# Kernel tuning notes

Hardware: AMD Instinct MI355X
Metric: run time of the kernel (lower is better)

The kernel has to match this reference:

```python
import math
import jax, jax.numpy as jnp
import numpy as np

DIM = 1280
NUM_HEADS = 16
HEAD_DIM = DIM // NUM_HEADS  # 80
N_SEG = 8
SEG_LEN = 1024
TOTAL = N_SEG * SEG_LEN  # 8192


def setup_inputs() -> dict:
    key = jax.random.key(0)
    ks = jax.random.split(key, 6)
    hidden_states = jax.random.normal(ks[0], (TOTAL, DIM), dtype=jnp.float32)
    # equal-length packed segments (8 images x 1024 patches)
    cu_seqlens = jnp.arange(N_SEG + 1, dtype=jnp.int32) * SEG_LEN
    rotary_pos_emb = jax.random.uniform(ks[1], (TOTAL, HEAD_DIM // 2), dtype=jnp.float32) * (2.0 * math.pi)
    s = 0.02
    qkv_w = jax.random.normal(ks[2], (DIM, 3 * DIM), dtype=jnp.float32) * s
    qkv_b = jnp.zeros((3 * DIM,), dtype=jnp.float32)
    proj_w = jax.random.normal(ks[3], (DIM, DIM), dtype=jnp.float32) * s
    proj_b = jnp.zeros((DIM,), dtype=jnp.float32)
    return {
        "hidden_states": hidden_states,
        "rotary_pos_emb": rotary_pos_emb,
        "qkv_w": qkv_w,
        "qkv_b": qkv_b,
        "proj_w": proj_w,
        "proj_b": proj_b,
        "cu_seqlens": cu_seqlens,
    }


def _rotate_half(x):
    d = x.shape[-1] // 2
    return jnp.concatenate([-x[..., d:], x[..., :d]], axis=-1)


def _apply_rope(t, freqs):
    # t: [S, H, D] ; freqs: [S, D/2]
    orig = t.dtype
    tf = t.astype(jnp.float32)
    cos = jnp.tile(jnp.cos(freqs), (1, 2))[:, None, :].astype(jnp.float32)  # [S,1,D]
    sin = jnp.tile(jnp.sin(freqs), (1, 2))[:, None, :].astype(jnp.float32)
    return (tf * cos + _rotate_half(tf) * sin).astype(orig)


def reference(hidden_states, rotary_pos_emb, qkv_w, qkv_b, proj_w, proj_b, cu_seqlens):
    S, dim = hidden_states.shape
    H, D = NUM_HEADS, HEAD_DIM
    n_seg = cu_seqlens.shape[0] - 1  # static
    L = S // n_seg  # equal-length segments

    qkv = hidden_states @ qkv_w + qkv_b            # [S, 3*dim]
    qkv = qkv.reshape(S, 3, H, D)
    q, k, v = qkv[:, 0], qkv[:, 1], qkv[:, 2]      # [S, H, D]

    q = _apply_rope(q, rotary_pos_emb)
    k = _apply_rope(k, rotary_pos_emb)

    # block-diagonal (per-segment) attention, vectorized over segments
    qs = q.reshape(n_seg, L, H, D).transpose(0, 2, 1, 3)  # [G,H,L,D]
    ks = k.reshape(n_seg, L, H, D).transpose(0, 2, 1, 3)
    vs = v.reshape(n_seg, L, H, D).transpose(0, 2, 1, 3)

    scale = 1.0 / math.sqrt(D)
    scores = jnp.einsum("ghld,ghmd->ghlm", qs, ks) * scale       # [G,H,L,L]
    probs = jax.nn.softmax(scores.astype(jnp.float32), axis=-1).astype(qs.dtype)
    out = jnp.einsum("ghlm,ghmd->ghld", probs, vs)               # [G,H,L,D]
    out = out.transpose(0, 2, 1, 3).reshape(S, H * D)            # [S, dim]
    return out @ proj_w + proj_b
```

## Files before the change

kernel.cpp:

```cpp
#include <hip/hip_runtime.h>
#include <hip/hip_bf16.h>
#include <math.h>

#define DIM 1280
#define NHEADS 16
#define HD 80
#define HDP 96
#define NSEG 8
#define SEGLEN 1024
#define TOTAL (NSEG*SEGLEN)

typedef unsigned short u16;
typedef __attribute__((ext_vector_type(8))) short bf16x8;
typedef __attribute__((ext_vector_type(4))) float f32x4;

__device__ __forceinline__ u16 f2b(float f) {
    union { float f; unsigned int i; } v; v.f = f;
    unsigned int x = v.i;
    unsigned int r = x + 0x7FFFu + ((x >> 16) & 1u);
    return (u16)(r >> 16);
}
__device__ __forceinline__ float b2f(u16 u) {
    union { unsigned int i; float f; } v; v.i = ((unsigned int)u) << 16;
    return v.f;
}
__device__ __forceinline__ void gload16(const u16* g, u16* l) {
    __builtin_amdgcn_global_load_lds(
        (const __attribute__((address_space(1))) unsigned int*)g,
        (__attribute__((address_space(3))) unsigned int*)l, 16, 0, 0);
}

__global__ __launch_bounds__(256) void cvt_f32_bf16(const float* __restrict__ in,
                                                    u16* __restrict__ out, int n4) {
    int i = blockIdx.x * 256 + threadIdx.x;
    if (i >= n4) return;
    float4 a = ((const float4*)in)[i];
    u16 o[4] = { f2b(a.x), f2b(a.y), f2b(a.z), f2b(a.w) };
    *(ulong1*)&out[i*4] = *(ulong1*)o;
}

__global__ __launch_bounds__(256) void cvtT_w(const float* __restrict__ in,
                                              u16* __restrict__ out, int K, int N) {
    __shared__ float t[32][33];
    const int kb = blockIdx.x * 32, nb = blockIdx.y * 32;
    const int tx = threadIdx.x & 31, ty = threadIdx.x >> 5;
    #pragma unroll
    for (int i = 0; i < 4; ++i) {
        int r = i*8 + ty;
        t[r][tx] = in[(size_t)(kb + r)*N + nb + tx];
    }
    __syncthreads();
    #pragma unroll
    for (int i = 0; i < 4; ++i) {
        int n = i*8 + ty;
        out[(size_t)(nb + n)*K + kb + tx] = f2b(t[tx][n]);
    }
}

template<int MODE>
__global__ __launch_bounds__(256) void gemm_bf16(
    const u16* __restrict__ A, const u16* __restrict__ BT,
    const float* __restrict__ bias,
    float* __restrict__ Cf, u16* __restrict__ qo, u16* __restrict__ ko,
    u16* __restrict__ vo, int M, int N, int K)
{
    __shared__ u16 sA[128*32];
    __shared__ u16 sB[128*32];
    const int tid = threadIdx.x;
    const int w = tid >> 6, l = tid & 63;
    const int lq = l & 15, lg = l >> 4;
    const int brow = blockIdx.y * 128, bcol = blockIdx.x * 128;
    const int wr = (w >> 1) * 64, wc = (w & 1) * 64;
    const int arow = w*32 + (l >> 2);
    const int acol = (l & 3) * 8;

    f32x4 acc[4][4] = {};

    for (int k0 = 0; k0 < K; k0 += 32) {
        __syncthreads();
        #pragma unroll
        for (int i = 0; i < 2; ++i) {
            gload16(A  + (size_t)(brow + arow + i*16)*K + k0 + acol, &sA[w*1024 + i*512]);
            gload16(BT + (size_t)(bcol + arow + i*16)*K + k0 + acol, &sB[w*1024 + i*512]);
        }
        __syncthreads();
        bf16x8 af[4], bfr[4];
        #pragma unroll
        for (int m = 0; m < 4; ++m) af[m]  = *(const bf16x8*)&sA[(wr + m*16 + lq)*32 + lg*8];
        #pragma unroll
        for (int n = 0; n < 4; ++n) bfr[n] = *(const bf16x8*)&sB[(wc + n*16 + lq)*32 + lg*8];
        #pragma unroll
        for (int m = 0; m < 4; ++m)
            #pragma unroll
            for (int n = 0; n < 4; ++n)
                acc[m][n] = __builtin_amdgcn_mfma_f32_16x16x32_bf16(af[m], bfr[n], acc[m][n], 0, 0, 0);
    }

    #pragma unroll
    for (int m = 0; m < 4; ++m) {
        #pragma unroll
        for (int n = 0; n < 4; ++n) {
            #pragma unroll
            for (int r = 0; r < 4; ++r) {
                const int row = brow + wr + m*16 + lg*4 + r;
                const int col = bcol + wc + n*16 + lq;
                float val = acc[m][n][r] + bias[col];
                if (MODE == 0) {
                    Cf[(size_t)row*N + col] = val;
                } else {
                    int part = col / DIM, rem = col - part*DIM;
                    int hh = rem / HD, dd = rem - hh*HD;
                    int g = row >> 10, ll = row & 1023;
                    size_t tok = (size_t)((g*NHEADS + hh)*SEGLEN + ll);
                    if      (part == 0) qo[tok*HDP + dd] = f2b(val);
                    else if (part == 1) ko[tok*HDP + dd] = f2b(val);
                    else                vo[tok*HD  + dd] = f2b(val);
                }
            }
        }
    }
}

__global__ __launch_bounds__(256) void rope_pad(u16* __restrict__ qb, u16* __restrict__ kb,
                                                const float* __restrict__ rp)
{
    int idx = blockIdx.x * 256 + threadIdx.x;
    int d = idx % 48;
    int t = idx / 48;
    int l = t & 1023, h = (t >> 10) & 15, g = t >> 14;
    size_t base = ((size_t)((g*NHEADS + h)*SEGLEN + l)) * HDP;
    if (d < 40) {
        float ang = rp[(size_t)(g*SEGLEN + l)*40 + d];
        float si, co;
        sincosf(ang, &si, &co);
        float q0 = b2f(qb[base + d]), q1 = b2f(qb[base + d + 40]);
        qb[base + d]      = f2b(q0*co - q1*si);
        qb[base + d + 40] = f2b(q1*co + q0*si);
        float k0 = b2f(kb[base + d]), k1 = b2f(kb[base + d + 40]);
        kb[base + d]      = f2b(k0*co - k1*si);
        kb[base + d + 40] = f2b(k1*co + k0*si);
    } else {
        int dz = d - 40;
        qb[base + 80 + dz] = 0; qb[base + 88 + dz] = 0;
        kb[base + 80 + dz] = 0; kb[base + 88 + dz] = 0;
    }
}

__global__ __launch_bounds__(256) void transpose_v(const u16* __restrict__ v,
                                                   u16* __restrict__ vt)
{
    __shared__ u16 sT[64][82];
    const int gh = blockIdx.y;
    const int st = blockIdx.x;
    const u16* src = v  + (size_t)gh*SEGLEN*HD + (size_t)st*64*HD;
    u16*       dst = vt + (size_t)gh*HD*SEGLEN + (size_t)st*64;
    const int tid = threadIdx.x;
    #pragma unroll
    for (int p = 0; p < 20; ++p) {
        int e = p*256 + tid;
        int r = e / 80, c = e - r*80;
        sT[r][c] = src[r*HD + c];
    }
    __syncthreads();
    #pragma unroll
    for (int p = 0; p < 20; ++p) {
        int e = p*256 + tid;
        int dd = e >> 6, s = e & 63;
        dst[(size_t)dd*SEGLEN + s] = sT[s][dd];
    }
}

__global__ __launch_bounds__(256) void attn_mfma(
    const u16* __restrict__ qb, const u16* __restrict__ kb,
    const u16* __restrict__ vt, u16* __restrict__ ob)
{
    const int qt = blockIdx.x;
    const int h  = blockIdx.y;
    const int g  = blockIdx.z;
    const float scale = 0.11180339887498949f;
    const float L2E = 1.4426950408889634f;

    __shared__ u16 sK[64*HDP];
    __shared__ u16 sVT[80][72];
    __shared__ u16 sP[4][16][72];

    const int tid = threadIdx.x;
    const int w = tid >> 6, l = tid & 63;
    const int lq = l & 15, lg = l >> 4;

    const size_t gh = (size_t)(g*NHEADS + h);
    const u16* Qg  = qb + gh*SEGLEN*HDP + (size_t)qt*64*HDP;
    const u16* Kg  = kb + gh*SEGLEN*HDP;
    const u16* VTg = vt + gh*HD*SEGLEN;

    bf16x8 qf[3];
    #pragma unroll
    for (int s = 0; s < 3; ++s)
        qf[s] = *(const bf16x8*)(Qg + (size_t)(w*16 + lq)*HDP + s*32 + lg*8);

    float m = -1e30f, lse = 0.f;
    f32x4 Oc[5] = {};

    for (int kt = 0; kt < 16; ++kt) {
        __syncthreads();
        #pragma unroll
        for (int i = 0; i < 3; ++i) {
            int o = (i*4 + w)*1024 + l*16;
            int row = o / 192, cc = (o % 192) >> 1;
            gload16(Kg + (size_t)(kt*64 + row)*HDP + cc, &sK[(i*4 + w)*512]);
        }
        #pragma unroll
        for (int p = 0; p < 3; ++p) {
            int c = p*256 + tid;
            if (c < 640) {
                int dd = c >> 3, s8 = (c & 7)*8;
                *(bf16x8*)&sVT[dd][s8] =
                    *(const bf16x8*)(VTg + (size_t)dd*SEGLEN + kt*64 + s8);
            }
        }
        __syncthreads();

        f32x4 sf[4];
        #pragma unroll
        for (int fi = 0; fi < 4; ++fi) {
            f32x4 c = {0.f, 0.f, 0.f, 0.f};
            #pragma unroll
            for (int s = 0; s < 3; ++s) {
                bf16x8 a = *(const bf16x8*)&sK[(fi*16 + lq)*HDP + s*32 + lg*8];
                c = __builtin_amdgcn_mfma_f32_16x16x32_bf16(a, qf[s], c, 0, 0, 0);
            }
            sf[fi] = c;
        }

        float sv[4][4];
        float rm = -1e30f;
        #pragma unroll
        for (int fi = 0; fi < 4; ++fi)
            #pragma unroll
            for (int r = 0; r < 4; ++r) {
                float x = sf[fi][r] * scale;
                sv[fi][r] = x;
                rm = fmaxf(rm, x);
            }
        rm = fmaxf(rm, __shfl_xor(rm, 16, 64));
        rm = fmaxf(rm, __shfl_xor(rm, 32, 64));
        float mnew = fmaxf(m, rm);
        float alpha = exp2f((m - mnew) * L2E);
        float psum = 0.f;
        #pragma unroll
        for (int fi = 0; fi < 4; ++fi)
            #pragma unroll
            for (int r = 0; r < 4; ++r) {
                float p = exp2f((sv[fi][r] - mnew) * L2E);
                sv[fi][r] = p;
                psum += p;
            }
        psum += __shfl_xor(psum, 16, 64);
        psum += __shfl_xor(psum, 32, 64);
        lse = lse * alpha + psum;
        m = mnew;

        #pragma unroll
        for (int fi = 0; fi < 4; ++fi) {
            unsigned int w0 = (unsigned int)f2b(sv[fi][0]) | ((unsigned int)f2b(sv[fi][1]) << 16);
            unsigned int w1 = (unsigned int)f2b(sv[fi][2]) | ((unsigned int)f2b(sv[fi][3]) << 16);
            uint2 val; val.x = w0; val.y = w1;
            *(uint2*)&sP[w][lq][fi*16 + lg*4] = val;
        }

        float a0 = __shfl(alpha, lg*4 + 0, 64);
        float a1 = __shfl(alpha, lg*4 + 1, 64);
        float a2 = __shfl(alpha, lg*4 + 2, 64);
        float a3 = __shfl(alpha, lg*4 + 3, 64);
        #pragma unroll
        for (int n = 0; n < 5; ++n) {
            Oc[n][0] *= a0; Oc[n][1] *= a1; Oc[n][2] *= a2; Oc[n][3] *= a3;
        }

        #pragma unroll
        for (int ks = 0; ks < 2; ++ks) {
            bf16x8 pa = *(const bf16x8*)&sP[w][lq][ks*32 + lg*8];
            #pragma unroll
            for (int n = 0; n < 5; ++n) {
                bf16x8 vb = *(const bf16x8*)&sVT[n*16 + lq][ks*32 + lg*8];
                Oc[n] = __builtin_amdgcn_mfma_f32_16x16x32_bf16(pa, vb, Oc[n], 0, 0, 0);
            }
        }
    }

    float inv = 1.f / lse;
    float i0 = __shfl(inv, lg*4 + 0, 64);
    float i1 = __shfl(inv, lg*4 + 1, 64);
    float i2 = __shfl(inv, lg*4 + 2, 64);
    float i3 = __shfl(inv, lg*4 + 3, 64);
    const float iv[4] = { i0, i1, i2, i3 };
    #pragma unroll
    for (int n = 0; n < 5; ++n) {
        #pragma unroll
        for (int r = 0; r < 4; ++r) {
            int tok = g*SEGLEN + qt*64 + w*16 + lg*4 + r;
            int col = h*HD + n*16 + lq;
            ob[(size_t)tok*DIM + col] = f2b(Oc[n][r] * iv[r]);
        }
    }
}

extern "C" void kernel_launch(void* const* d_in, const int* in_sizes, int n_in,
                              void* d_out, int out_size, void* d_ws, size_t ws_size,
                              hipStream_t stream) {
    const float* hs     = (const float*)d_in[0];
    const float* rope   = (const float*)d_in[1];
    const float* qkv_w  = (const float*)d_in[2];
    const float* qkv_b  = (const float*)d_in[3];
    const float* proj_w = (const float*)d_in[4];
    const float* proj_b = (const float*)d_in[5];

    char* ws = (char*)d_ws;
    u16* hsb    = (u16*)(ws);
    u16* wqkvt  = (u16*)(ws + 20971520);
    u16* wprojt = (u16*)(ws + 30801920);
    u16* qpad   = (u16*)(ws + 34078720);
    u16* kpad   = (u16*)(ws + 59244544);
    u16* vbuf   = (u16*)(ws + 84410368);
    u16* vtb    = (u16*)(ws + 105381888);
    u16* obb    = (u16*)(ws + 126353408);

    cvt_f32_bf16<<<(TOTAL*DIM/4 + 255)/256, 256, 0, stream>>>(hs, hsb, TOTAL*DIM/4);
    cvtT_w<<<dim3(DIM/32, 3*DIM/32), 256, 0, stream>>>(qkv_w, wqkvt, DIM, 3*DIM);
    cvtT_w<<<dim3(DIM/32, DIM/32), 256, 0, stream>>>(proj_w, wprojt, DIM, DIM);

    gemm_bf16<1><<<dim3(3*DIM/128, TOTAL/128), 256, 0, stream>>>(
        hsb, wqkvt, qkv_b, nullptr, qpad, kpad, vbuf, TOTAL, 3*DIM, DIM);

    rope_pad<<<NSEG*NHEADS*SEGLEN*48/256, 256, 0, stream>>>(qpad, kpad, rope);

    transpose_v<<<dim3(SEGLEN/64, NSEG*NHEADS), 256, 0, stream>>>(vbuf, vtb);

    attn_mfma<<<dim3(SEGLEN/64, NHEADS, NSEG), 256, 0, stream>>>(qpad, kpad, vtb, obb);

    gemm_bf16<0><<<dim3(DIM/128, TOTAL/128), 256, 0, stream>>>(
        obb, wprojt, proj_b, (float*)d_out, nullptr, nullptr, nullptr, TOTAL, DIM, DIM);
}
```

Before: 441.5 us.

## Replace GEMMs with 256x256 double-buffered swizzled kernel; precompute rope sincos table

Replaces the 128x128 single-buffered bf16 GEMM with a 512-thread 256x256 tile kernel. It uses a 64-wide K step, double-buffered LDS with staged prefetch, XOR-swizzled LDS layout, s_setprio around MFMA bursts, and an XCD-aware block remap. RoPE now reads a precomputed cos/sin table built by a separate kernel and processes a whole token per thread with vectorized loads. This targets global-memory latency and LDS bank conflicts in the GEMMs. In exchange it uses much more shared memory per block, and the table aliases the attention-output buffer, which is safe only because of launch ordering.

```diff
diff --git a/kernel.cpp b/kernel.cpp
--- a/kernel.cpp
+++ b/kernel.cpp
@@ -57,54 +57,151 @@
     }
 }
 
+__global__ __launch_bounds__(256) void ctab_build(const float* __restrict__ rp,
+                                                  float2* __restrict__ cs) {
+    int i = blockIdx.x * 256 + threadIdx.x;
+    if (i >= TOTAL*40) return;
+    float s, c;
+    sincosf(rp[i], &s, &c);
+    cs[i] = make_float2(c, s);
+}
+
 template<int MODE>
-__global__ __launch_bounds__(256) void gemm_bf16(
+__global__ __launch_bounds__(512, 2) void gemm8p(
     const u16* __restrict__ A, const u16* __restrict__ BT,
     const float* __restrict__ bias,
     float* __restrict__ Cf, u16* __restrict__ qo, u16* __restrict__ ko,
-    u16* __restrict__ vo, int M, int N, int K)
+    u16* __restrict__ vo, int M, int N, int K, int nbx)
 {
-    __shared__ u16 sA[128*32];
-    __shared__ u16 sB[128*32];
+    __shared__ u16 sA[2][256*64];
+    __shared__ u16 sB[2][256*64];
+
     const int tid = threadIdx.x;
     const int w = tid >> 6, l = tid & 63;
     const int lq = l & 15, lg = l >> 4;
-    const int brow = blockIdx.y * 128, bcol = blockIdx.x * 128;
-    const int wr = (w >> 1) * 64, wc = (w & 1) * 64;
-    const int arow = w*32 + (l >> 2);
-    const int acol = (l & 3) * 8;
-
-    f32x4 acc[4][4] = {};
-
-    for (int k0 = 0; k0 < K; k0 += 32) {
-        __syncthreads();
-        #pragma unroll
-        for (int i = 0; i < 2; ++i) {
-            gload16(A  + (size_t)(brow + arow + i*16)*K + k0 + acol, &sA[w*1024 + i*512]);
-            gload16(BT + (size_t)(bcol + arow + i*16)*K + k0 + acol, &sB[w*1024 + i*512]);
-        }
-        __syncthreads();
-        bf16x8 af[4], bfr[4];
-        #pragma unroll
-        for (int m = 0; m < 4; ++m) af[m]  = *(const bf16x8*)&sA[(wr + m*16 + lq)*32 + lg*8];
-        #pragma unroll
-        for (int n = 0; n < 4; ++n) bfr[n] = *(const bf16x8*)&sB[(wc + n*16 + lq)*32 + lg*8];
-        #pragma unroll
-        for (int m = 0; m < 4; ++m)
+    const int wm = w >> 2, wn = w & 3;
+
+    const int nwg = gridDim.x;
+    const int q8 = nwg >> 3;
+    const int id = blockIdx.x;
+    const int id2 = (id & 7) * q8 + (id >> 3);
+    const int bx = id2 % nbx, by = id2 / nbx;
+    const int brow = by * 256, bcol = bx * 256;
+
+    const int rlo  = w*8 + (l >> 3);
+    const int srcc = (l & 7) ^ ((l >> 3) & 7);
+    const size_t aBase = (size_t)(brow + rlo)*K + srcc*8;
+    const size_t bBase = (size_t)(bcol + rlo)*K + srcc*8;
+
+    const int cx0 = (0 + lg) ^ (lq & 7);
+    const int cx1 = (4 + lg) ^ (lq & 7);
+
+    f32x4 acc[8][4] = {};
+    const int NT = K >> 6;
+
+    u16* cA = &sA[0][0]; u16* cB = &sB[0][0];
+    u16* nA = &sA[1][0]; u16* nB = &sB[1][0];
+
+    #pragma unroll
+    for (int ci = 0; ci < 4; ++ci) {
+        gload16(A  + aBase + (size_t)(ci*64)*K, &cA[(ci*512 + w*64)*8]);
+        gload16(BT + bBase + (size_t)(ci*64)*K, &cB[(ci*512 + w*64)*8]);
+    }
+    asm volatile("s_waitcnt vmcnt(0)" ::: "memory");
+    __builtin_amdgcn_s_barrier();
+
+    for (int t = 0; t < NT; ++t) {
+        const bool pf = (t + 1 < NT);
+        const int kb = (t + 1) << 6;
+        bf16x8 af[4], bf[4];
+
+        if (pf) {
+            gload16(A  + aBase + (size_t)(0*64)*K + kb, &nA[(0*512 + w*64)*8]);
+            gload16(A  + aBase + (size_t)(2*64)*K + kb, &nA[(2*512 + w*64)*8]);
+            gload16(BT + bBase + (size_t)(0*64)*K + kb, &nB[(0*512 + w*64)*8]);
+        }
+        #pragma unroll
+        for (int n = 0; n < 4; ++n)
+            bf[n] = *(const bf16x8*)&cB[(wn*64 + n*16 + lq)*64 + cx0*8];
+        #pragma unroll
+        for (int mi = 0; mi < 4; ++mi)
+            af[mi] = *(const bf16x8*)&cA[(wm*128 + mi*16 + lq)*64 + cx0*8];
+        __builtin_amdgcn_s_barrier();
+        __builtin_amdgcn_s_setprio(1);
+        #pragma unroll
+        for (int mi = 0; mi < 4; ++mi)
             #pragma unroll
             for (int n = 0; n < 4; ++n)
-                acc[m][n] = __builtin_amdgcn_mfma_f32_16x16x32_bf16(af[m], bfr[n], acc[m][n], 0, 0, 0);
-    }
-
-    #pragma unroll
-    for (int m = 0; m < 4; ++m) {
+                acc[mi][n] = __builtin_amdgcn_mfma_f32_16x16x32_bf16(af[mi], bf[n], acc[mi][n], 0, 0, 0);
+        __builtin_amdgcn_s_setprio(0);
+        __builtin_amdgcn_s_barrier();
+
+        if (pf) {
+            gload16(A  + aBase + (size_t)(1*64)*K + kb, &nA[(1*512 + w*64)*8]);
+            gload16(A  + aBase + (size_t)(3*64)*K + kb, &nA[(3*512 + w*64)*8]);
+            gload16(BT + bBase + (size_t)(1*64)*K + kb, &nB[(1*512 + w*64)*8]);
+        }
+        #pragma unroll
+        for (int mi = 0; mi < 4; ++mi)
+            af[mi] = *(const bf16x8*)&cA[(wm*128 + 64 + mi*16 + lq)*64 + cx0*8];
+        __builtin_amdgcn_s_barrier();
+        __builtin_amdgcn_s_setprio(1);
+        #pragma unroll
+        for (int mi = 0; mi < 4; ++mi)
+            #pragma unroll
+            for (int n = 0; n < 4; ++n)
+                acc[4+mi][n] = __builtin_amdgcn_mfma_f32_16x16x32_bf16(af[mi], bf[n], acc[4+mi][n], 0, 0, 0);
+        __builtin_amdgcn_s_setprio(0);
+        __builtin_amdgcn_s_barrier();
+
+        if (pf) {
+            gload16(BT + bBase + (size_t)(2*64)*K + kb, &nB[(2*512 + w*64)*8]);
+            gload16(BT + bBase + (size_t)(3*64)*K + kb, &nB[(3*512 + w*64)*8]);
+        }
+        #pragma unroll
+        for (int n = 0; n < 4; ++n)
+            bf[n] = *(const bf16x8*)&cB[(wn*64 + n*16 + lq)*64 + cx1*8];
+        #pragma unroll
+        for (int mi = 0; mi < 4; ++mi)
+            af[mi] = *(const bf16x8*)&cA[(wm*128 + mi*16 + lq)*64 + cx1*8];
+        __builtin_amdgcn_s_barrier();
+        __builtin_amdgcn_s_setprio(1);
+        #pragma unroll
+        for (int mi = 0; mi < 4; ++mi)
+            #pragma unroll
+            for (int n = 0; n < 4; ++n)
+                acc[mi][n] = __builtin_amdgcn_mfma_f32_16x16x32_bf16(af[mi], bf[n], acc[mi][n], 0, 0, 0);
+        __builtin_amdgcn_s_setprio(0);
+        __builtin_amdgcn_s_barrier();
+
+        #pragma unroll
+        for (int mi = 0; mi < 4; ++mi)
+            af[mi] = *(const bf16x8*)&cA[(wm*128 + 64 + mi*16 + lq)*64 + cx1*8];
+        __builtin_amdgcn_s_barrier();
+        __builtin_amdgcn_s_setprio(1);
+        #pragma unroll
+        for (int mi = 0; mi < 4; ++mi)
+            #pragma unroll
+            for (int n = 0; n < 4; ++n)
+                acc[4+mi][n] = __builtin_amdgcn_mfma_f32_16x16x32_bf16(af[mi], bf[n], acc[4+mi][n], 0, 0, 0);
+        __builtin_amdgcn_s_setprio(0);
+        if (pf) asm volatile("s_waitcnt vmcnt(0)" ::: "memory");
+        __builtin_amdgcn_s_barrier();
+
+        u16* tA = cA; cA = nA; nA = tA;
+        u16* tB = cB; cB = nB; nB = tB;
+    }
+
+    #pragma unroll
+    for (int mf = 0; mf < 8; ++mf) {
         #pragma unroll
         for (int n = 0; n < 4; ++n) {
+            const int col = bcol + wn*64 + n*16 + lq;
+            const float bv = bias[col];
             #pragma unroll
             for (int r = 0; r < 4; ++r) {
-                const int row = brow + wr + m*16 + lg*4 + r;
-                const int col = bcol + wc + n*16 + lq;
-                float val = acc[m][n][r] + bias[col];
+                const int row = brow + wm*128 + mf*16 + lg*4 + r;
+                float val = acc[mf][n][r] + bv;
                 if (MODE == 0) {
                     Cf[(size_t)row*N + col] = val;
                 } else {
@@ -121,29 +218,43 @@
     }
 }
 
-__global__ __launch_bounds__(256) void rope_pad(u16* __restrict__ qb, u16* __restrict__ kb,
-                                                const float* __restrict__ rp)
+__global__ __launch_bounds__(256) void rope_pad2(u16* __restrict__ qb, u16* __restrict__ kb,
+                                                 const float2* __restrict__ cs)
 {
     int idx = blockIdx.x * 256 + threadIdx.x;
-    int d = idx % 48;
-    int t = idx / 48;
-    int l = t & 1023, h = (t >> 10) & 15, g = t >> 14;
+    int l = idx & 1023, h = (idx >> 10) & 15, g = idx >> 14;
     size_t base = ((size_t)((g*NHEADS + h)*SEGLEN + l)) * HDP;
-    if (d < 40) {
-        float ang = rp[(size_t)(g*SEGLEN + l)*40 + d];
-        float si, co;
-        sincosf(ang, &si, &co);
-        float q0 = b2f(qb[base + d]), q1 = b2f(qb[base + d + 40]);
-        qb[base + d]      = f2b(q0*co - q1*si);
-        qb[base + d + 40] = f2b(q1*co + q0*si);
-        float k0 = b2f(kb[base + d]), k1 = b2f(kb[base + d + 40]);
-        kb[base + d]      = f2b(k0*co - k1*si);
-        kb[base + d + 40] = f2b(k1*co + k0*si);
-    } else {
-        int dz = d - 40;
-        qb[base + 80 + dz] = 0; qb[base + 88 + dz] = 0;
-        kb[base + 80 + dz] = 0; kb[base + 88 + dz] = 0;
-    }
+    const float2* c0 = cs + (size_t)(g*SEGLEN + l) * 40;
+    #pragma unroll
+    for (int p = 0; p < 5; ++p) {
+        float cv[8], sv[8];
+        #pragma unroll
+        for (int j2 = 0; j2 < 4; ++j2) {
+            float4 f = ((const float4*)(c0 + p*8))[j2];
+            cv[j2*2] = f.x; sv[j2*2] = f.y; cv[j2*2+1] = f.z; sv[j2*2+1] = f.w;
+        }
+        bf16x8 qlo = *(const bf16x8*)&qb[base + p*8];
+        bf16x8 qhi = *(const bf16x8*)&qb[base + 40 + p*8];
+        bf16x8 klo = *(const bf16x8*)&kb[base + p*8];
+        bf16x8 khi = *(const bf16x8*)&kb[base + 40 + p*8];
+        bf16x8 qlo2, qhi2, klo2, khi2;
+        #pragma unroll
+        for (int j = 0; j < 8; ++j) {
+            float a  = b2f((u16)qlo[j]), b  = b2f((u16)qhi[j]);
+            qlo2[j] = (short)f2b(a*cv[j]  - b*sv[j]);
+            qhi2[j] = (short)f2b(b*cv[j]  + a*sv[j]);
+            float ka = b2f((u16)klo[j]), kb2 = b2f((u16)khi[j]);
+            klo2[j] = (short)f2b(ka*cv[j] - kb2*sv[j]);
+            khi2[j] = (short)f2b(kb2*cv[j] + ka*sv[j]);
+        }
+        *(bf16x8*)&qb[base + p*8]      = qlo2;
+        *(bf16x8*)&qb[base + 40 + p*8] = qhi2;
+        *(bf16x8*)&kb[base + p*8]      = klo2;
+        *(bf16x8*)&kb[base + 40 + p*8] = khi2;
+    }
+    bf16x8 z = {};
+    *(bf16x8*)&qb[base + 80] = z; *(bf16x8*)&qb[base + 88] = z;
+    *(bf16x8*)&kb[base + 80] = z; *(bf16x8*)&kb[base + 88] = z;
 }
 
 __global__ __launch_bounds__(256) void transpose_v(const u16* __restrict__ v,
@@ -324,20 +435,22 @@
     u16* vbuf   = (u16*)(ws + 84410368);
     u16* vtb    = (u16*)(ws + 105381888);
     u16* obb    = (u16*)(ws + 126353408);
+    float2* ctab = (float2*)(ws + 126353408);
 
     cvt_f32_bf16<<<(TOTAL*DIM/4 + 255)/256, 256, 0, stream>>>(hs, hsb, TOTAL*DIM/4);
     cvtT_w<<<dim3(DIM/32, 3*DIM/32), 256, 0, stream>>>(qkv_w, wqkvt, DIM, 3*DIM);
     cvtT_w<<<dim3(DIM/32, DIM/32), 256, 0, stream>>>(proj_w, wprojt, DIM, DIM);
-
-    gemm_bf16<1><<<dim3(3*DIM/128, TOTAL/128), 256, 0, stream>>>(
-        hsb, wqkvt, qkv_b, nullptr, qpad, kpad, vbuf, TOTAL, 3*DIM, DIM);
-
-    rope_pad<<<NSEG*NHEADS*SEGLEN*48/256, 256, 0, stream>>>(qpad, kpad, rope);
+    ctab_build<<<(TOTAL*40 + 255)/256, 256, 0, stream>>>(rope, ctab);
+
+    gemm8p<1><<<dim3((3*DIM/256) * (TOTAL/256)), 512, 0, stream>>>(
+        hsb, wqkvt, qkv_b, nullptr, qpad, kpad, vbuf, TOTAL, 3*DIM, DIM, 3*DIM/256);
+
+    rope_pad2<<<NSEG*NHEADS*SEGLEN/256, 256, 0, stream>>>(qpad, kpad, ctab);
 
     transpose_v<<<dim3(SEGLEN/64, NSEG*NHEADS), 256, 0, stream>>>(vbuf, vtb);
 
     attn_mfma<<<dim3(SEGLEN/64, NHEADS, NSEG), 256, 0, stream>>>(qpad, kpad, vtb, obb);
 
-    gemm_bf16<0><<<dim3(DIM/128, TOTAL/128), 256, 0, stream>>>(
-        obb, wprojt, proj_b, (float*)d_out, nullptr, nullptr, nullptr, TOTAL, DIM, DIM);
-}
+    gemm8p<0><<<dim3((DIM/256) * (TOTAL/256)), 512, 0, stream>>>(
+        obb, wprojt, proj_b, (float*)d_out, nullptr, nullptr, nullptr, TOTAL, DIM, DIM, DIM/256);
+}
```

New measurement: 441.7 us. No clear change (+0.0%).
